# Kernel tuning notes

Measured on AMD Instinct MI355X. Metric: run time of the kernel, lower is better.

Reference implementation:

```python
import jax, jax.numpy as jnp
import numpy as np
from jax.ops import segment_sum

N_NODES = 100000
N_EDGES = 3200000
N_GRAPHS = 64


def gcn_conv(x, W, b, src, dst, n_nodes):
    # Linear transform first (PyG GCNConv applies lin before propagate)
    h = x @ W  # [N, out]
    # Add self loops
    loop = jnp.arange(n_nodes, dtype=src.dtype)
    s = jnp.concatenate([src, loop])
    d = jnp.concatenate([dst, loop])
    # Symmetric normalization deg^-1/2 (deg counts incoming edges incl. self loop)
    deg = segment_sum(jnp.ones_like(d, dtype=h.dtype), d, num_segments=n_nodes)
    dinv = jnp.where(deg > 0, jax.lax.rsqrt(deg), 0.0)
    norm = dinv[s] * dinv[d]  # [E+N]
    # Gather messages from source, scale, scatter-add to target
    msg = h[s] * norm[:, None]
    out = segment_sum(msg, d, num_segments=n_nodes)
    return out + b


def setup_inputs() -> dict:
    key = jax.random.key(0)
    ks = jax.random.split(key, 6)
    x = jax.random.normal(ks[0], (N_NODES, 128), dtype=jnp.float32)
    edge_index = jax.random.randint(ks[1], (2, N_EDGES), 0, N_NODES, dtype=jnp.int64)
    batch = jnp.sort(jax.random.randint(ks[2], (N_NODES,), 0, N_GRAPHS, dtype=jnp.int64))
    W1 = jax.random.normal(ks[3], (128, 256), dtype=jnp.float32) * (1.0 / np.sqrt(128))
    b1 = jnp.zeros((256,), dtype=jnp.float32)
    W2 = jax.random.normal(ks[4], (256, 128), dtype=jnp.float32) * (1.0 / np.sqrt(256))
    b2 = jnp.zeros((128,), dtype=jnp.float32)
    return {"x": x, "edge_index": edge_index, "batch": batch,
            "W1": W1, "b1": b1, "W2": W2, "b2": b2, "num_graphs": N_GRAPHS}


def reference(x, edge_index, batch, W1, b1, W2, b2, num_graphs):
    n_nodes = x.shape[0]
    src, dst = edge_index[0], edge_index[1]
    # dropout(p=0.6, training=False) is identity at inference
    h = jax.nn.relu(gcn_conv(x, W1, b1, src, dst, n_nodes))
    h = gcn_conv(h, W2, b2, src, dst, n_nodes)
    # global_mean_pool by graph id
    sums = segment_sum(h, batch, num_segments=num_graphs)
    counts = segment_sum(jnp.ones((n_nodes,), dtype=h.dtype), batch, num_segments=num_graphs)
    return sums / jnp.maximum(counts, 1.0)[:, None]
```

## Files before the change

### kernel.cpp

```cpp
#include <hip/hip_runtime.h>
#include <hip/hip_bf16.h>
#include <stdint.h>

#define N_NODES 100000
#define N_EDGES 3200000
#define N_GRAPHS 64
#define BSH 7
#define NBK 128
#define NB 782
#define G_SC 512
#define EPB 6250

typedef unsigned int u32;
typedef unsigned short u16;
typedef __attribute__((ext_vector_type(8))) short bf16x8;
typedef __attribute__((ext_vector_type(4))) float f32x4;

__device__ __forceinline__ float bf_lo(u32 u){ return __uint_as_float(u << 16); }
__device__ __forceinline__ float bf_hi(u32 u){ return __uint_as_float(u & 0xffff0000u); }
__device__ __forceinline__ u16 f2bf(float f){
    union { __hip_bfloat16 h; u16 u; } c; c.h = __float2bfloat16(f); return c.u;
}
__device__ __forceinline__ u32 pack2(float a, float b){
    return (u32)f2bf(a) | ((u32)f2bf(b) << 16);
}

__global__ __launch_bounds__(512) void k_hist(const int* __restrict__ dst,
                                              int* __restrict__ hist){
    __shared__ int h[NB];
    int tid = threadIdx.x, g = blockIdx.x;
    for (int i = tid; i < NB; i += 512) h[i] = 0;
    __syncthreads();
    const int2* d2 = reinterpret_cast<const int2*>(dst + g * EPB);
    for (int i = tid; i < EPB / 2; i += 512){
        int2 d = d2[i];
        atomicAdd(&h[d.x >> BSH], 1);
        atomicAdd(&h[d.y >> BSH], 1);
    }
    __syncthreads();
    for (int i = tid; i < NB; i += 512) hist[i * G_SC + g] = h[i];
}

__global__ __launch_bounds__(512) void k_colscan(const int* __restrict__ hist,
                                                 int* __restrict__ cursors,
                                                 int* __restrict__ btot){
    __shared__ int sm[512];
    int b = blockIdx.x, tid = threadIdx.x;
    int v = hist[b * G_SC + tid];
    sm[tid] = v; __syncthreads();
    for (int off = 1; off < 512; off <<= 1){
        int t = (tid >= off) ? sm[tid - off] : 0;
        __syncthreads(); sm[tid] += t; __syncthreads();
    }
    cursors[b * G_SC + tid] = sm[tid] - v;
    if (tid == 511) btot[b] = sm[511];
}

__global__ __launch_bounds__(1024) void k_bscan(const int* __restrict__ btot,
                                                int* __restrict__ bbase){
    __shared__ int sm[1024];
    int tid = threadIdx.x;
    int v = (tid < NB) ? btot[tid] : 0;
    sm[tid] = v; __syncthreads();
    for (int off = 1; off < 1024; off <<= 1){
        int t = (tid >= off) ? sm[tid - off] : 0;
        __syncthreads(); sm[tid] += t; __syncthreads();
    }
    if (tid < NB) bbase[tid] = sm[tid] - v;
    if (tid == 0) bbase[NB] = N_EDGES;
}

__global__ __launch_bounds__(512) void k_scatter(const int* __restrict__ src,
                                                 const int* __restrict__ dst,
                                                 const int* __restrict__ cursors,
                                                 const int* __restrict__ bbase,
                                                 u32* __restrict__ pairs){
    __shared__ int cur[NB];
    int g = blockIdx.x, tid = threadIdx.x;
    for (int i = tid; i < NB; i += 512) cur[i] = cursors[i * G_SC + g] + bbase[i];
    __syncthreads();
    const int2* s2 = reinterpret_cast<const int2*>(src + g * EPB);
    const int2* d2 = reinterpret_cast<const int2*>(dst + g * EPB);
    for (int i = tid; i < EPB / 2; i += 512){
        int2 s = s2[i]; int2 d = d2[i];
        int p0 = atomicAdd(&cur[d.x >> BSH], 1);
        pairs[p0] = (u32)s.x | ((u32)(d.x & (NBK - 1)) << 24);
        int p1 = atomicAdd(&cur[d.y >> BSH], 1);
        pairs[p1] = (u32)s.y | ((u32)(d.y & (NBK - 1)) << 24);
    }
}

__global__ __launch_bounds__(512) void k_fine(const u32* __restrict__ pairs,
                                              const int* __restrict__ bbase,
                                              int* __restrict__ offsets,
                                              float* __restrict__ dinv,
                                              int* __restrict__ csr_src){
    __shared__ int ldeg[NBK];
    __shared__ int ssc[NBK];
    __shared__ int lcur[NBK];
    int b = blockIdx.x, tid = threadIdx.x;
    int node0 = b << BSH;
    if (tid < NBK) ldeg[tid] = 0;
    __syncthreads();
    int e0 = bbase[b], e1 = bbase[b + 1];
    for (int e = e0 + tid; e < e1; e += 512)
        atomicAdd(&ldeg[pairs[e] >> 24], 1);
    __syncthreads();
    int myDeg = (tid < NBK) ? ldeg[tid] : 0;
    if (tid < NBK) ssc[tid] = myDeg;
    __syncthreads();
    for (int off = 1; off < NBK; off <<= 1){
        int t = 0;
        if (tid >= off && tid < NBK) t = ssc[tid - off];
        __syncthreads();
        if (tid < NBK) ssc[tid] += t;
        __syncthreads();
    }
    if (tid < NBK){
        int excl = ssc[tid] - myDeg;
        int n = node0 + tid;
        if (n <= N_NODES) offsets[n] = e0 + excl;
        if (n < N_NODES)  dinv[n] = rsqrtf((float)myDeg + 1.0f);
        lcur[tid] = e0 + excl;
    }
    __syncthreads();
    for (int e = e0 + tid; e < e1; e += 512){
        u32 p = pairs[e];
        int pos = atomicAdd(&lcur[p >> 24], 1);
        csr_src[pos] = (int)(p & 0xFFFFFFu);
    }
}

__global__ void k_cvt_x(const float* __restrict__ x, const float* __restrict__ dinv,
                        u32* __restrict__ xb){
    int i = blockIdx.x * blockDim.x + threadIdx.x;
    if (i < N_NODES * 32){
        float w = dinv[i >> 5];
        float4 f = reinterpret_cast<const float4*>(x)[i];
        uint2 p = make_uint2(pack2(f.x * w, f.y * w), pack2(f.z * w, f.w * w));
        reinterpret_cast<uint2*>(xb)[i] = p;
    }
}

__global__ void k_cvt_w(const float* __restrict__ W1, const float* __restrict__ W2,
                        u16* __restrict__ w1t, u16* __restrict__ w2t){
    int i = blockIdx.x * blockDim.x + threadIdx.x;
    if (i < 128 * 256){
        int n = i / 128, k = i % 128;
        w1t[i] = f2bf(W1[k * 256 + n]);
    } else {
        int j = i - 128 * 256;
        int n = j / 256, k = j % 256;
        w2t[j] = f2bf(W2[k * 128 + n]);
    }
}

__global__ __launch_bounds__(256) void k_agg(const u32* __restrict__ X,
                      const int* __restrict__ offs, const int* __restrict__ csr_src,
                      const float* __restrict__ dinv, u32* __restrict__ out){
    int lane = threadIdx.x & 63;
    int v = blockIdx.x * 4 + (threadIdx.x >> 6);
    u32 u = X[v * 64 + lane];
    float a0 = bf_lo(u), a1 = bf_hi(u);
    int e1 = offs[v + 1];
    for (int e = offs[v]; e < e1; e += 64){
        int idx = e + lane;
        int sv = (idx < e1) ? csr_src[idx] : 0;
        int cnt = min(64, e1 - e);
        int j = 0;
        for (; j + 8 <= cnt; j += 8){
            int s0 = __shfl(sv, j),   s1 = __shfl(sv, j+1), s2 = __shfl(sv, j+2), s3 = __shfl(sv, j+3);
            int s4 = __shfl(sv, j+4), s5 = __shfl(sv, j+5), s6 = __shfl(sv, j+6), s7 = __shfl(sv, j+7);
            u32 u0 = X[s0*64 + lane], u1 = X[s1*64 + lane], u2 = X[s2*64 + lane], u3 = X[s3*64 + lane];
            u32 u4 = X[s4*64 + lane], u5 = X[s5*64 + lane], u6 = X[s6*64 + lane], u7 = X[s7*64 + lane];
            a0 += (bf_lo(u0) + bf_lo(u1)) + (bf_lo(u2) + bf_lo(u3))
                + (bf_lo(u4) + bf_lo(u5)) + (bf_lo(u6) + bf_lo(u7));
            a1 += (bf_hi(u0) + bf_hi(u1)) + (bf_hi(u2) + bf_hi(u3))
                + (bf_hi(u4) + bf_hi(u5)) + (bf_hi(u6) + bf_hi(u7));
        }
        for (; j < cnt; j++){
            int s = __shfl(sv, j);
            u32 uu = X[s*64 + lane];
            a0 += bf_lo(uu); a1 += bf_hi(uu);
        }
    }
    float w = dinv[v];
    out[v*64 + lane] = pack2(a0 * w, a1 * w);
}

template<int BK, int BN, bool RELU, bool BIAS, bool SCALE>
__global__ __launch_bounds__(256) void k_gemm(const u16* __restrict__ A, const u16* __restrict__ BT,
                        const float* __restrict__ bias, const float* __restrict__ rowscale,
                        u16* __restrict__ C, int M){
    __shared__ char As[64 * BK * 2];
    const int tid = threadIdx.x;
    const int rowbytes = BK * 2;
    const int units = 8 * BK;
    for (int it = tid; it < units; it += 256){
        int flat = it * 16;
        int r = flat / rowbytes, cb = flat % rowbytes;
        int grow = blockIdx.x * 64 + r;
        int4 val = make_int4(0,0,0,0);
        if (grow < M) val = *reinterpret_cast<const int4*>(A + (size_t)grow * BK + cb / 2);
        *reinterpret_cast<int4*>(As + r * rowbytes + (cb ^ ((r & 7) << 4))) = val;
    }
    __syncthreads();

    const int wid = tid >> 6, lane = tid & 63;
    const int r0 = wid * 16;
    constexpr int NF = BN / 16;
    f32x4 acc[NF];
#pragma unroll
    for (int i = 0; i < NF; i++) acc[i] = (f32x4){0.f,0.f,0.f,0.f};
    const int ar = r0 + (lane & 15);
    const int koff = (lane >> 4) * 8;
#pragma unroll
    for (int kb = 0; kb < BK / 32; kb++){
        int kbyte = (kb * 32 + koff) * 2;
        bf16x8 aF = *reinterpret_cast<const bf16x8*>(As + ar * rowbytes + (kbyte ^ ((ar & 7) << 4)));
#pragma unroll
        for (int nf = 0; nf < NF; nf++){
            int bn = nf * 16 + (lane & 15);
            bf16x8 bF = *reinterpret_cast<const bf16x8*>(BT + bn * BK + kb * 32 + koff);
            acc[nf] = __builtin_amdgcn_mfma_f32_16x16x32_bf16(aF, bF, acc[nf], 0, 0, 0);
        }
    }
#pragma unroll
    for (int nf = 0; nf < NF; nf++){
        int col = nf * 16 + (lane & 15);
        float bv = BIAS ? bias[col] : 0.f;
#pragma unroll
        for (int j = 0; j < 4; j++){
            int grow = blockIdx.x * 64 + r0 + (lane >> 4) * 4 + j;
            if (grow < M){
                float val = acc[nf][j] + bv;
                if (RELU) val = fmaxf(val, 0.f);
                if (SCALE) val *= rowscale[grow];
                C[(size_t)grow * BN + col] = f2bf(val);
            }
        }
    }
}

__global__ void k_pool(const u32* __restrict__ t2, const int* __restrict__ batch,
                       float* __restrict__ psum, float* __restrict__ counts){
    const int NPB = 100;
    int n0 = blockIdx.x * NPB, n1 = min(n0 + NPB, N_NODES);
    int tid = threadIdx.x;
    float r0 = 0.f, r1 = 0.f; int gcur = batch[n0]; int runlen = 0;
    for (int n = n0; n < n1; n++){
        int g = batch[n];
        if (g != gcur){
            atomicAdd(&psum[gcur * 128 + 2 * tid], r0);
            atomicAdd(&psum[gcur * 128 + 2 * tid + 1], r1);
            if (tid == 0) atomicAdd(&counts[gcur], (float)runlen);
            r0 = 0.f; r1 = 0.f; runlen = 0; gcur = g;
        }
        u32 u = t2[(size_t)n * 64 + tid];
        r0 += bf_lo(u); r1 += bf_hi(u);
        runlen++;
    }
    atomicAdd(&psum[gcur * 128 + 2 * tid], r0);
    atomicAdd(&psum[gcur * 128 + 2 * tid + 1], r1);
    if (tid == 0) atomicAdd(&counts[gcur], (float)runlen);
}

__global__ void k_final(const float* __restrict__ psum, const float* __restrict__ counts,
                        const float* __restrict__ b2, float* __restrict__ out){
    int g = blockIdx.x, c = threadIdx.x;
    out[g * 128 + c] = psum[g * 128 + c] / fmaxf(counts[g], 1.0f) + b2[c];
}

extern "C" void kernel_launch(void* const* d_in, const int* in_sizes, int n_in,
                              void* d_out, int out_size, void* d_ws, size_t ws_size,
                              hipStream_t stream){
    const float* x   = (const float*)d_in[0];
    const int*   ei  = (const int*)d_in[1];
    const int* batch = (const int*)d_in[2];
    const float* W1  = (const float*)d_in[3];
    const float* b1  = (const float*)d_in[4];
    const float* W2  = (const float*)d_in[5];
    const float* b2  = (const float*)d_in[6];
    float* out = (float*)d_out;
    const int* esrc = ei;
    const int* edst = ei + N_EDGES;

    char* w = (char*)d_ws;
    size_t off = 0;
    auto alloc = [&](size_t bytes) -> char* {
        char* p = w + off; off += (bytes + 255) & ~size_t(255); return p;
    };
    float* dinv     = (float*)alloc((size_t)N_NODES * 4);
    int*   offsets  = (int*)  alloc((size_t)(N_NODES + 1) * 4);
    int*   hist     = (int*)  alloc((size_t)NB * G_SC * 4);
    int*   cursors  = (int*)  alloc((size_t)NB * G_SC * 4);
    int*   btot     = (int*)  alloc((size_t)NB * 4);
    int*   bbase    = (int*)  alloc((size_t)(NB + 1) * 4);
    int*   csr_src  = (int*)  alloc((size_t)N_EDGES * 4);
    u32*   xb       = (u32*)  alloc((size_t)N_NODES * 64 * 4);
    u16*   aggx     = (u16*)  alloc((size_t)N_NODES * 128 * 2);
    u16*   h        = (u16*)  alloc((size_t)N_NODES * 256 * 2);
    u16*   t        = (u16*)  alloc((size_t)N_NODES * 128 * 2);
    u16*   w1t      = (u16*)  alloc(128 * 256 * 2);
    u16*   w2t      = (u16*)  alloc(256 * 128 * 2);
    float* psum     = (float*)alloc((size_t)N_GRAPHS * 128 * 4);
    float* counts   = (float*)alloc((size_t)N_GRAPHS * 4);
    u32*   t2       = (u32*)h;
    u32*   pairs    = (u32*)h;

    hipMemsetAsync(psum, 0, (size_t)N_GRAPHS * 128 * 4, stream);
    hipMemsetAsync(counts, 0, (size_t)N_GRAPHS * 4, stream);

    k_hist   <<<G_SC, 512, 0, stream>>>(edst, hist);
    k_colscan<<<NB, 512, 0, stream>>>(hist, cursors, btot);
    k_bscan  <<<1, 1024, 0, stream>>>(btot, bbase);
    k_scatter<<<G_SC, 512, 0, stream>>>(esrc, edst, cursors, bbase, pairs);
    k_fine   <<<NB, 512, 0, stream>>>(pairs, bbase, offsets, dinv, csr_src);

    k_cvt_x<<<12500, 256, 0, stream>>>(x, dinv, xb);
    k_cvt_w<<<256, 256, 0, stream>>>(W1, W2, w1t, w2t);

    k_agg<<<25000, 256, 0, stream>>>(xb, offsets, csr_src, dinv, (u32*)aggx);
    k_gemm<128, 256, true, true, false><<<1563, 256, 0, stream>>>(
        aggx, w1t, b1, nullptr, h, N_NODES);
    k_gemm<256, 128, false, false, true><<<1563, 256, 0, stream>>>(
        h, w2t, nullptr, dinv, t, N_NODES);
    k_agg<<<25000, 256, 0, stream>>>((const u32*)t, offsets, csr_src, dinv, t2);
    k_pool <<<1000, 64, 0, stream>>>(t2, batch, psum, counts);
    k_final<<<N_GRAPHS, 128, 0, stream>>>(psum, counts, b2, out);
}
```

Measured before the change: 610.8 us.

## Fuse both GEMMs through LDS, merge prep kernels, widen CSR buckets

Fuses the two dense GEMMs into a single kernel that keeps the 64x256 ReLU hidden tile in shared memory, so the hidden activation never goes to global memory. Merges the x and weight conversion kernels into one launch, folds the psum/counts zeroing into the histogram kernel in place of the memsets, and doubles the coarse bucket width (fewer buckets, smaller scan). This removes about 50MB of global traffic and several launches. In exchange the fused kernel uses 48KB of LDS per block, which may lower occupancy, and each fine-sort block now handles 256 nodes.

```diff
diff --git a/kernel.cpp b/kernel.cpp
--- a/kernel.cpp
+++ b/kernel.cpp
@@ -5,9 +5,9 @@
 #define N_NODES 100000
 #define N_EDGES 3200000
 #define N_GRAPHS 64
-#define BSH 7
-#define NBK 128
-#define NB 782
+#define BSH 8
+#define NBK 256
+#define NB 391
 #define G_SC 512
 #define EPB 6250
 
@@ -26,9 +26,15 @@
 }
 
 __global__ __launch_bounds__(512) void k_hist(const int* __restrict__ dst,
-                                              int* __restrict__ hist){
+                                              int* __restrict__ hist,
+                                              float* __restrict__ psum,
+                                              float* __restrict__ counts){
     __shared__ int h[NB];
     int tid = threadIdx.x, g = blockIdx.x;
+    if (g == 0){
+        for (int i = tid; i < N_GRAPHS * 128; i += 512) psum[i] = 0.f;
+        if (tid < N_GRAPHS) counts[tid] = 0.f;
+    }
     for (int i = tid; i < NB; i += 512) h[i] = 0;
     __syncthreads();
     const int2* d2 = reinterpret_cast<const int2*>(dst + g * EPB);
@@ -56,13 +62,13 @@
     if (tid == 511) btot[b] = sm[511];
 }
 
-__global__ __launch_bounds__(1024) void k_bscan(const int* __restrict__ btot,
-                                                int* __restrict__ bbase){
-    __shared__ int sm[1024];
+__global__ __launch_bounds__(512) void k_bscan(const int* __restrict__ btot,
+                                               int* __restrict__ bbase){
+    __shared__ int sm[512];
     int tid = threadIdx.x;
     int v = (tid < NB) ? btot[tid] : 0;
     sm[tid] = v; __syncthreads();
-    for (int off = 1; off < 1024; off <<= 1){
+    for (int off = 1; off < 512; off <<= 1){
         int t = (tid >= off) ? sm[tid - off] : 0;
         __syncthreads(); sm[tid] += t; __syncthreads();
     }
@@ -131,27 +137,27 @@
     }
 }
 
-__global__ void k_cvt_x(const float* __restrict__ x, const float* __restrict__ dinv,
-                        u32* __restrict__ xb){
-    int i = blockIdx.x * blockDim.x + threadIdx.x;
-    if (i < N_NODES * 32){
+__global__ void k_prep(const float* __restrict__ x, const float* __restrict__ dinv,
+                       u32* __restrict__ xb,
+                       const float* __restrict__ W1, const float* __restrict__ W2,
+                       u16* __restrict__ w1t, u16* __restrict__ w2t){
+    int bid = blockIdx.x;
+    if (bid < 12500){
+        int i = bid * 256 + threadIdx.x;
         float w = dinv[i >> 5];
         float4 f = reinterpret_cast<const float4*>(x)[i];
         uint2 p = make_uint2(pack2(f.x * w, f.y * w), pack2(f.z * w, f.w * w));
         reinterpret_cast<uint2*>(xb)[i] = p;
-    }
-}
-
-__global__ void k_cvt_w(const float* __restrict__ W1, const float* __restrict__ W2,
-                        u16* __restrict__ w1t, u16* __restrict__ w2t){
-    int i = blockIdx.x * blockDim.x + threadIdx.x;
-    if (i < 128 * 256){
-        int n = i / 128, k = i % 128;
-        w1t[i] = f2bf(W1[k * 256 + n]);
     } else {
-        int j = i - 128 * 256;
-        int n = j / 256, k = j % 256;
-        w2t[j] = f2bf(W2[k * 128 + n]);
+        int i = (bid - 12500) * 256 + threadIdx.x;
+        if (i < 128 * 256){
+            int n = i / 128, k = i % 128;
+            w1t[i] = f2bf(W1[k * 256 + n]);
+        } else {
+            int j = i - 128 * 256;
+            int n = j / 256, k = j % 256;
+            w2t[j] = f2bf(W2[k * 128 + n]);
+        }
     }
 }
 
@@ -188,55 +194,82 @@
     out[v*64 + lane] = pack2(a0 * w, a1 * w);
 }
 
-template<int BK, int BN, bool RELU, bool BIAS, bool SCALE>
-__global__ __launch_bounds__(256) void k_gemm(const u16* __restrict__ A, const u16* __restrict__ BT,
-                        const float* __restrict__ bias, const float* __restrict__ rowscale,
+__global__ __launch_bounds__(256) void k_mlp(const u16* __restrict__ A,
+                        const u16* __restrict__ B1T, const u16* __restrict__ B2T,
+                        const float* __restrict__ b1, const float* __restrict__ dinv,
                         u16* __restrict__ C, int M){
-    __shared__ char As[64 * BK * 2];
+    __shared__ char As[64 * 256];
+    __shared__ char C1[64 * 512];
     const int tid = threadIdx.x;
-    const int rowbytes = BK * 2;
-    const int units = 8 * BK;
-    for (int it = tid; it < units; it += 256){
+    for (int it = tid; it < 1024; it += 256){
         int flat = it * 16;
-        int r = flat / rowbytes, cb = flat % rowbytes;
+        int r = flat >> 8, cb = flat & 255;
         int grow = blockIdx.x * 64 + r;
         int4 val = make_int4(0,0,0,0);
-        if (grow < M) val = *reinterpret_cast<const int4*>(A + (size_t)grow * BK + cb / 2);
-        *reinterpret_cast<int4*>(As + r * rowbytes + (cb ^ ((r & 7) << 4))) = val;
+        if (grow < M) val = *reinterpret_cast<const int4*>(A + (size_t)grow * 128 + cb / 2);
+        *reinterpret_cast<int4*>(As + r * 256 + (cb ^ ((r & 7) << 4))) = val;
     }
     __syncthreads();
 
     const int wid = tid >> 6, lane = tid & 63;
     const int r0 = wid * 16;
-    constexpr int NF = BN / 16;
-    f32x4 acc[NF];
-#pragma unroll
-    for (int i = 0; i < NF; i++) acc[i] = (f32x4){0.f,0.f,0.f,0.f};
     const int ar = r0 + (lane & 15);
     const int koff = (lane >> 4) * 8;
-#pragma unroll
-    for (int kb = 0; kb < BK / 32; kb++){
-        int kbyte = (kb * 32 + koff) * 2;
-        bf16x8 aF = *reinterpret_cast<const bf16x8*>(As + ar * rowbytes + (kbyte ^ ((ar & 7) << 4)));
-#pragma unroll
-        for (int nf = 0; nf < NF; nf++){
-            int bn = nf * 16 + (lane & 15);
-            bf16x8 bF = *reinterpret_cast<const bf16x8*>(BT + bn * BK + kb * 32 + koff);
-            acc[nf] = __builtin_amdgcn_mfma_f32_16x16x32_bf16(aF, bF, acc[nf], 0, 0, 0);
-        }
-    }
-#pragma unroll
-    for (int nf = 0; nf < NF; nf++){
-        int col = nf * 16 + (lane & 15);
-        float bv = BIAS ? bias[col] : 0.f;
+    {
+        f32x4 acc[16];
+#pragma unroll
+        for (int i = 0; i < 16; i++) acc[i] = (f32x4){0.f,0.f,0.f,0.f};
+#pragma unroll
+        for (int kb = 0; kb < 4; kb++){
+            int kbyte = (kb * 32 + koff) * 2;
+            bf16x8 aF = *reinterpret_cast<const bf16x8*>(As + ar * 256 + (kbyte ^ ((ar & 7) << 4)));
+#pragma unroll
+            for (int nf = 0; nf < 16; nf++){
+                int bn = nf * 16 + (lane & 15);
+                bf16x8 bF = *reinterpret_cast<const bf16x8*>(B1T + bn * 128 + kb * 32 + koff);
+                acc[nf] = __builtin_amdgcn_mfma_f32_16x16x32_bf16(aF, bF, acc[nf], 0, 0, 0);
+            }
+        }
+#pragma unroll
+        for (int nf = 0; nf < 16; nf++){
+            int col = nf * 16 + (lane & 15);
+            float bv = b1[col];
+#pragma unroll
+            for (int j = 0; j < 4; j++){
+                int r = r0 + (lane >> 4) * 4 + j;
+                float val = fmaxf(acc[nf][j] + bv, 0.f);
+                *reinterpret_cast<u16*>(C1 + r * 512 + ((col * 2) ^ ((r & 7) << 4))) = f2bf(val);
+            }
+        }
+    }
+    __syncthreads();
+    {
+        f32x4 acc[8];
+#pragma unroll
+        for (int i = 0; i < 8; i++) acc[i] = (f32x4){0.f,0.f,0.f,0.f};
+#pragma unroll
+        for (int kb = 0; kb < 8; kb++){
+            int kbyte = (kb * 32 + koff) * 2;
+            bf16x8 aF = *reinterpret_cast<const bf16x8*>(C1 + ar * 512 + (kbyte ^ ((ar & 7) << 4)));
+#pragma unroll
+            for (int nf = 0; nf < 8; nf++){
+                int bn = nf * 16 + (lane & 15);
+                bf16x8 bF = *reinterpret_cast<const bf16x8*>(B2T + bn * 256 + kb * 32 + koff);
+                acc[nf] = __builtin_amdgcn_mfma_f32_16x16x32_bf16(aF, bF, acc[nf], 0, 0, 0);
+            }
+        }
+        float dj[4]; int gr[4];
 #pragma unroll
         for (int j = 0; j < 4; j++){
-            int grow = blockIdx.x * 64 + r0 + (lane >> 4) * 4 + j;
-            if (grow < M){
-                float val = acc[nf][j] + bv;
-                if (RELU) val = fmaxf(val, 0.f);
-                if (SCALE) val *= rowscale[grow];
-                C[(size_t)grow * BN + col] = f2bf(val);
+            gr[j] = blockIdx.x * 64 + r0 + (lane >> 4) * 4 + j;
+            dj[j] = (gr[j] < M) ? dinv[gr[j]] : 0.f;
+        }
+#pragma unroll
+        for (int nf = 0; nf < 8; nf++){
+            int col = nf * 16 + (lane & 15);
+#pragma unroll
+            for (int j = 0; j < 4; j++){
+                if (gr[j] < M) C[(size_t)gr[j] * 128 + col] = f2bf(acc[nf][j] * dj[j]);
             }
         }
     }
@@ -297,34 +330,26 @@
     int*   btot     = (int*)  alloc((size_t)NB * 4);
     int*   bbase    = (int*)  alloc((size_t)(NB + 1) * 4);
     int*   csr_src  = (int*)  alloc((size_t)N_EDGES * 4);
+    u32*   pairs    = (u32*)  alloc((size_t)N_EDGES * 4);
     u32*   xb       = (u32*)  alloc((size_t)N_NODES * 64 * 4);
     u16*   aggx     = (u16*)  alloc((size_t)N_NODES * 128 * 2);
-    u16*   h        = (u16*)  alloc((size_t)N_NODES * 256 * 2);
     u16*   t        = (u16*)  alloc((size_t)N_NODES * 128 * 2);
+    u32*   t2       = (u32*)  alloc((size_t)N_NODES * 64 * 4);
     u16*   w1t      = (u16*)  alloc(128 * 256 * 2);
     u16*   w2t      = (u16*)  alloc(256 * 128 * 2);
     float* psum     = (float*)alloc((size_t)N_GRAPHS * 128 * 4);
     float* counts   = (float*)alloc((size_t)N_GRAPHS * 4);
-    u32*   t2       = (u32*)h;
-    u32*   pairs    = (u32*)h;
-
-    hipMemsetAsync(psum, 0, (size_t)N_GRAPHS * 128 * 4, stream);
-    hipMemsetAsync(counts, 0, (size_t)N_GRAPHS * 4, stream);
-
-    k_hist   <<<G_SC, 512, 0, stream>>>(edst, hist);
+
+    k_hist   <<<G_SC, 512, 0, stream>>>(edst, hist, psum, counts);
     k_colscan<<<NB, 512, 0, stream>>>(hist, cursors, btot);
-    k_bscan  <<<1, 1024, 0, stream>>>(btot, bbase);
+    k_bscan  <<<1, 512, 0, stream>>>(btot, bbase);
     k_scatter<<<G_SC, 512, 0, stream>>>(esrc, edst, cursors, bbase, pairs);
     k_fine   <<<NB, 512, 0, stream>>>(pairs, bbase, offsets, dinv, csr_src);
 
-    k_cvt_x<<<12500, 256, 0, stream>>>(x, dinv, xb);
-    k_cvt_w<<<256, 256, 0, stream>>>(W1, W2, w1t, w2t);
+    k_prep<<<12756, 256, 0, stream>>>(x, dinv, xb, W1, W2, w1t, w2t);
 
     k_agg<<<25000, 256, 0, stream>>>(xb, offsets, csr_src, dinv, (u32*)aggx);
-    k_gemm<128, 256, true, true, false><<<1563, 256, 0, stream>>>(
-        aggx, w1t, b1, nullptr, h, N_NODES);
-    k_gemm<256, 128, false, false, true><<<1563, 256, 0, stream>>>(
-        h, w2t, nullptr, dinv, t, N_NODES);
+    k_mlp<<<1563, 256, 0, stream>>>(aggx, w1t, w2t, b1, dinv, t, N_NODES);
     k_agg<<<25000, 256, 0, stream>>>((const u32*)t, offsets, csr_src, dinv, t2);
     k_pool <<<1000, 64, 0, stream>>>(t2, batch, psum, counts);
     k_final<<<N_GRAPHS, 128, 0, stream>>>(psum, counts, b2, out);
```

After: 547.6 us. 10.4% less time.
